# Kernel tuning notes

Measured on AMD Instinct MI355X. Metric: run time of the kernel, lower is better.

The kernel has to match this reference:

```python
import jax, jax.numpy as jnp
import numpy as np

N_FFT = 4096
HOP = 1024
WIN = 300          # wiener_win_len (frames per independent Wiener chunk)
EPS = 1e-10
SCALE_FACTOR = 10.0


def hann(n):
    # torch.hann_window (periodic)
    return 0.5 * (1.0 - jnp.cos(2.0 * jnp.pi * jnp.arange(n) / n))


def stft(x, window):
    # x: (N, C, T) -> complex (N, C, B, F), center=True, reflect pad, onesided
    pad = N_FFT // 2
    xp = jnp.pad(x, ((0, 0), (0, 0), (pad, pad)), mode='reflect')
    n_frames = 1 + (xp.shape[-1] - N_FFT) // HOP
    idx = jnp.arange(n_frames)[:, None] * HOP + jnp.arange(N_FFT)[None, :]
    frames = xp[..., idx] * window                      # (N,C,F,n_fft)
    spec = jnp.fft.rfft(frames, axis=-1)                # (N,C,F,B)
    return jnp.swapaxes(spec, -1, -2)                   # (N,C,B,F)


def istft(spec, window, length):
    # spec: (..., B, F) complex -> (..., length) real; center=True inverse
    frames = jnp.fft.irfft(jnp.swapaxes(spec, -1, -2), n=N_FFT, axis=-1) * window
    n_frames = frames.shape[-2]
    out_len = N_FFT + HOP * (n_frames - 1)
    idx = jnp.arange(n_frames)[:, None] * HOP + jnp.arange(N_FFT)[None, :]
    out = jnp.zeros(frames.shape[:-2] + (out_len,), frames.dtype).at[..., idx].add(frames)
    wsum = jnp.zeros((out_len,), frames.dtype).at[idx].add(
        jnp.broadcast_to(window ** 2, idx.shape))
    out = out / jnp.where(wsum > 1e-11, wsum, 1.0)
    pad = N_FFT // 2
    return out[..., pad:pad + length]


def wiener_chunk(v, x, niter):
    # openunmix.filtering.wiener (softmask=False, residual=False) on one chunk.
    # v: (T, B, C, S) real target magnitudes; x: (T, B, C) complex mix STFT.
    phase = jnp.exp(1j * jnp.angle(x))                  # mixture phase init
    y = (v * phase[..., None]).astype(jnp.complex64)    # (T,B,C,S)
    max_abs = jnp.maximum(1.0, jnp.max(jnp.abs(x)) / SCALE_FACTOR)
    x = x / max_abs
    y = y / max_abs
    C = x.shape[-1]
    reg = np.sqrt(EPS) * jnp.eye(C, dtype=jnp.complex64)
    for _ in range(niter):  # expectation_maximization, one pass per iter
        psd = jnp.mean(jnp.abs(y) ** 2, axis=2)         # (T,B,S) channel-avg PSD
        # spatial covariance per bin/source, normalized by eps + sum_t psd
        R = jnp.einsum('tbcs,tbds->bcds', y, jnp.conj(y))
        R = R / (EPS + jnp.sum(psd, axis=0))[:, None, None, :]
        Cxx = reg + jnp.einsum('tbs,bcds->tbcd', psd.astype(jnp.complex64), R)
        inv = jnp.linalg.inv(Cxx)                       # (T,B,C,C)
        gain = jnp.einsum('bacs,tbcd->tbads', R, inv) * psd[:, :, None, None, :]
        y = jnp.einsum('tbacs,tbc->tbas', gain, x)      # (T,B,C,S)
    return y * max_abs


def setup_inputs() -> dict:
    key = jax.random.key(0)
    k1, k2 = jax.random.split(key)
    audio = jax.random.normal(k1, (2, 2, 613376), dtype=jnp.float32)
    W = jax.random.normal(k2, (4, 2049), dtype=jnp.float32)  # per-target per-bin mask logits
    return {'audio': audio, 'W': W, 'niter': 1}


def reference(audio, W, niter):
    window = hann(N_FFT).astype(audio.dtype)
    mix = stft(audio, window)                           # (N,C,B,F) complex
    X = jnp.abs(mix)                                    # ComplexNorm power=1
    # target models (stand-in: per-bin sigmoid masks); input detached as in torch
    Xd = jax.lax.stop_gradient(X)
    masks = jax.nn.sigmoid(W)                           # (S,B)
    specs = Xd[..., None] * jnp.transpose(masks)[None, None, :, None, :]  # (N,C,B,F,S)
    v = jnp.transpose(specs, (0, 3, 2, 1, 4))           # (N,F,B,C,S)
    xm = jnp.transpose(mix, (0, 3, 2, 1))               # (N,F,B,C)
    N, F, B, C = xm.shape
    S = v.shape[-1]
    n_chunks = F // WIN
    vc = v.reshape(N, n_chunks, WIN, B, C, S)
    xc = xm.reshape(N, n_chunks, WIN, B, C)
    wfun = lambda vv, xx: wiener_chunk(vv, xx, niter)
    yc = jax.vmap(jax.vmap(wfun))(vc, xc)               # (N,chunks,T,B,C,S)
    y = yc.reshape(N, F, B, C, S)
    y = jnp.transpose(y, (0, 4, 3, 2, 1))               # (N,S,C,B,F)
    estimates = istft(y, window, audio.shape[-1])       # (N,S,C,T)
    return estimates
```

## Files before the change

kernel.cpp:

```cpp
#include <hip/hip_runtime.h>
#include <math.h>

#define TLEN 613376
#define OLEN 617472
#define NFR  600
#define NB   2049
#define PI_F  3.14159265358979323846f
#define PI2_F 6.28318530717958647693f
#define PHYS(i) ((i) + ((i) >> 4))

__device__ __forceinline__ float winf(int j) {
  return 0.5f - 0.5f * __cosf(1.5339807878856412e-3f * (float)j);
}

__device__ __forceinline__ float wsum_at(int m) {
  int f_max = m >> 10; if (f_max > 599) f_max = 599;
  int f_min = (m - 3072) >> 10; if (f_min < 0) f_min = 0;
  float ws = 0.f;
  for (int f2 = f_min; f2 <= f_max; ++f2) {
    float w = winf(m - (f2 << 10));
    ws += w * w;
  }
  return (ws > 1e-11f) ? ws : 1.0f;
}

__device__ __forceinline__ float reflect_load(const float* __restrict__ x, int pos) {
  int k = pos - 2048;
  if (k < 0) k = -k;
  else if (k >= TLEN) k = 2 * TLEN - 2 - k;
  return x[k];
}

__device__ __forceinline__ float2 cmul(float2 a, float2 b) {
  return make_float2(a.x * b.x - a.y * b.y, a.x * b.y + a.y * b.x);
}
__device__ __forceinline__ float2 cadd(float2 a, float2 b) { return make_float2(a.x + b.x, a.y + b.y); }
__device__ __forceinline__ float2 csub(float2 a, float2 b) { return make_float2(a.x - b.x, a.y - b.y); }
template<int SGN>
__device__ __forceinline__ float2 muli(float2 a) {
  return (SGN > 0) ? make_float2(-a.y, a.x) : make_float2(a.y, -a.x);
}

template<int SGN>
__device__ __forceinline__ void fft4(float2 v[4]) {
  float2 t0 = cadd(v[0], v[2]), t1 = csub(v[0], v[2]);
  float2 t2 = cadd(v[1], v[3]), t3 = csub(v[1], v[3]);
  float2 it3 = muli<SGN>(t3);
  v[0] = cadd(t0, t2); v[2] = csub(t0, t2);
  v[1] = cadd(t1, it3); v[3] = csub(t1, it3);
}

template<int SGN>
__device__ __forceinline__ void fft8(float2 v[8]) {
  const float C = 0.70710678118654752440f;
  const float s = (SGN > 0) ? 1.0f : -1.0f;
  float2 t0 = cadd(v[0], v[4]), t1 = csub(v[0], v[4]);
  float2 t2 = cadd(v[2], v[6]), t3 = csub(v[2], v[6]);
  float2 e0 = cadd(t0, t2), e2 = csub(t0, t2);
  float2 it3 = muli<SGN>(t3);
  float2 e1 = cadd(t1, it3), e3 = csub(t1, it3);
  t0 = cadd(v[1], v[5]); t1 = csub(v[1], v[5]);
  t2 = cadd(v[3], v[7]); t3 = csub(v[3], v[7]);
  float2 o0 = cadd(t0, t2), o2 = csub(t0, t2);
  it3 = muli<SGN>(t3);
  float2 o1 = cadd(t1, it3), o3 = csub(t1, it3);
  float2 o1w = make_float2(C * (o1.x - s * o1.y), C * (o1.y + s * o1.x));
  float2 o2w = muli<SGN>(o2);
  float2 o3w = make_float2(C * (-o3.x - s * o3.y), C * (-o3.y + s * o3.x));
  v[0] = cadd(e0, o0);  v[4] = csub(e0, o0);
  v[1] = cadd(e1, o1w); v[5] = csub(e1, o1w);
  v[2] = cadd(e2, o2w); v[6] = csub(e2, o2w);
  v[3] = cadd(e3, o3w); v[7] = csub(e3, o3w);
}

template<int SGN>
__device__ __forceinline__ void twiddle8(float2 v[8], float ang) {
  float sn, cs;
  __sincosf((SGN > 0) ? ang : -ang, &sn, &cs);
  float2 w1 = make_float2(cs, sn);
  float2 w = w1;
  v[1] = cmul(v[1], w);
#pragma unroll
  for (int r = 2; r < 8; ++r) { w = cmul(w, w1); v[r] = cmul(v[r], w); }
}

template<int SGN>
__device__ __forceinline__ void fft2048_mid(float2* lds, float2 v[8], int tid) {
  fft8<SGN>(v);
#pragma unroll
  for (int r = 0; r < 8; ++r) { int i = tid * 8 + r; lds[PHYS(i)] = v[r]; }
  __syncthreads();
#pragma unroll
  for (int r = 0; r < 8; ++r) v[r] = lds[PHYS(tid + 256 * r)];
  twiddle8<SGN>(v, PI2_F * (1.0f / 64.0f) * (float)(tid & 7));
  fft8<SGN>(v);
  __syncthreads();
#pragma unroll
  for (int r = 0; r < 8; ++r) { int i = ((tid >> 3) << 6) + (tid & 7) + 8 * r; lds[PHYS(i)] = v[r]; }
  __syncthreads();
#pragma unroll
  for (int r = 0; r < 8; ++r) v[r] = lds[PHYS(tid + 256 * r)];
  twiddle8<SGN>(v, PI2_F * (1.0f / 512.0f) * (float)(tid & 63));
  fft8<SGN>(v);
  __syncthreads();
#pragma unroll
  for (int r = 0; r < 8; ++r) { int i = ((tid >> 6) << 9) + (tid & 63) + 64 * r; lds[PHYS(i)] = v[r]; }
  __syncthreads();
}

template<int SGN>
__device__ __forceinline__ void fft2048_last(const float2* lds, int jj, float2 u[4]) {
#pragma unroll
  for (int r = 0; r < 4; ++r) u[r] = lds[PHYS(jj + 512 * r)];
  float sn, cs;
  float ang = PI2_F * (1.0f / 2048.0f) * (float)jj;
  __sincosf((SGN > 0) ? ang : -ang, &sn, &cs);
  float2 w1 = make_float2(cs, sn);
  float2 w2 = cmul(w1, w1);
  float2 w3 = cmul(w2, w1);
  u[1] = cmul(u[1], w1); u[2] = cmul(u[2], w2); u[3] = cmul(u[3], w3);
  fft4<SGN>(u);
}

__global__ __launch_bounds__(256, 6) void stft_kernel(const float* __restrict__ audio,
                                                      float2* __restrict__ X) {
  __shared__ float2 lds[2176];
  int bid = blockIdx.x;
  int f  = bid % NFR;
  int nc = bid / NFR;
  const float* x = audio + (size_t)nc * TLEN;
  int tid = threadIdx.x;
  int base = f * 1024;
  float2 v[8];
#pragma unroll
  for (int r = 0; r < 8; ++r) {
    int k = tid + 256 * r;
    int j0 = 2 * k;
    v[r] = make_float2(reflect_load(x, base + j0)     * winf(j0),
                       reflect_load(x, base + j0 + 1) * winf(j0 + 1));
  }
  fft2048_mid<-1>(lds, v, tid);
  fft2048_last<-1>(lds, tid,        v);
  fft2048_last<-1>(lds, tid + 256,  v + 4);
  __syncthreads();
#pragma unroll
  for (int r = 0; r < 4; ++r) lds[PHYS(tid + 512 * r)] = v[r];
#pragma unroll
  for (int r = 0; r < 4; ++r) lds[PHYS(tid + 256 + 512 * r)] = v[4 + r];
  __syncthreads();
  float2* out = X + (size_t)bid * NB;
  float sn0, cs0;
  __sincosf(-PI_F * (float)tid * (1.0f / 2048.0f), &sn0, &cs0);
  float2 ph = make_float2(cs0, sn0);
  const float2 rot = make_float2(0.92387953251128675613f, -0.38268343236508977173f);
#pragma unroll
  for (int r = 0; r < 9; ++r) {
    int k = tid + 256 * r;
    if (k <= 2048) {
      float2 Zk = lds[PHYS(k & 2047)];
      float2 Zm = lds[PHYS((2048 - k) & 2047)];
      float Ex = 0.5f * (Zk.x + Zm.x), Ey = 0.5f * (Zk.y - Zm.y);
      float Dx = 0.5f * (Zk.x - Zm.x), Dy = 0.5f * (Zk.y + Zm.y);
      float Ox = Dy, Oy = -Dx;
      out[k] = make_float2(Ex + Ox * ph.x - Oy * ph.y, Ey + Ox * ph.y + Oy * ph.x);
    }
    ph = cmul(ph, rot);
  }
}

__global__ __launch_bounds__(256) void stats_kernel(const float2* __restrict__ X,
                                                    float* __restrict__ stats4,
                                                    unsigned int* __restrict__ maxsq) {
  __shared__ unsigned int sm;
  if (threadIdx.x == 0) sm = 0u;
  __syncthreads();
  int b = blockIdx.x * 256 + threadIdx.x;
  bool ok = (b < NB);
  int g = blockIdx.y;
  int n = g >> 1, chunk = g & 1;
  int t0 = blockIdx.z * 75;
  const float2* X0 = X + ((size_t)(n * 2 + 0) * NFR + chunk * 300 + t0) * NB + (ok ? b : 0);
  const float2* X1 = X + ((size_t)(n * 2 + 1) * NFR + chunk * 300 + t0) * NB + (ok ? b : 0);
  float s00 = 0.f, s11 = 0.f, sre = 0.f, sim = 0.f, lmax = 0.f;
  if (ok) {
    for (int t = 0; t < 75; ++t) {
      float2 a = X0[(size_t)t * NB];
      float2 c = X1[(size_t)t * NB];
      float pa = a.x * a.x + a.y * a.y;
      float pc = c.x * c.x + c.y * c.y;
      s00 += pa; s11 += pc;
      sre += a.x * c.x + a.y * c.y;
      sim += a.y * c.x - a.x * c.y;
      lmax = fmaxf(lmax, fmaxf(pa, pc));
    }
  }
  atomicMax(&sm, __float_as_uint(lmax));
  __syncthreads();
  if (threadIdx.x == 0) atomicMax(&maxsq[g], sm);
  if (ok) {
    float* sp = stats4 + ((size_t)g * NB + b) * 4;
    unsafeAtomicAdd(sp + 0, s00);
    unsafeAtomicAdd(sp + 1, s11);
    unsafeAtomicAdd(sp + 2, sre);
    unsafeAtomicAdd(sp + 3, sim);
  }
}

__global__ __launch_bounds__(256) void alpha_kernel(const float* __restrict__ Wmask,
                                                    const float4* __restrict__ stats4,
                                                    const unsigned int* __restrict__ maxsq,
                                                    float* __restrict__ alpha,
                                                    float* __restrict__ Ksum) {
  int idx = blockIdx.x * 256 + threadIdx.x;
  if (idx >= 4 * NB) return;
  int b = idx % NB;
  int g = idx / NB;
  float ma2 = fmaxf(1.0f, __uint_as_float(maxsq[g]) * 0.01f);
  float4 s4 = stats4[(size_t)g * NB + b];
  float P = 0.5f * (s4.x + s4.y) / ma2;
  float K = 0.f;
#pragma unroll
  for (int s = 0; s < 4; ++s) {
    float mv = 1.0f / (1.0f + expf(-Wmask[s * NB + b]));
    float m2 = mv * mv;
    float a = (m2 * m2) / (1e-10f + m2 * P);
    alpha[(size_t)(g * 4 + s) * NB + b] = a;
    K += a;
  }
  Ksum[(size_t)g * NB + b] = K;
}

__device__ __forceinline__ float2 wiener_eval(int b, const float2* __restrict__ x0row,
                                              const float2* __restrict__ x1row,
                                              const float4* __restrict__ srow,
                                              const float* __restrict__ arow,
                                              const float* __restrict__ krow,
                                              float ima2, int c) {
  float4 s4 = srow[b];
  float g00 = s4.x * ima2, g11 = s4.y * ima2, gre = s4.z * ima2, gim = s4.w * ima2;
  float K = krow[b];
  float as = arow[b];
  float2 x0 = x0row[b], x1 = x1row[b];
  float ph = 0.5f * ((x0.x * x0.x + x0.y * x0.y) + (x1.x * x1.x + x1.y * x1.y)) * ima2;
  float pk = ph * K;
  float M00 = 1e-5f + pk * g00;
  float M11 = 1e-5f + pk * g11;
  float Mre = pk * gre, Mim = pk * gim;
  float det = M00 * M11 - (Mre * Mre + Mim * Mim);
  float sc = ph * as / det;
  float u0x = M11 * x0.x - (Mre * x1.x - Mim * x1.y);
  float u0y = M11 * x0.y - (Mre * x1.y + Mim * x1.x);
  float u1x = M00 * x1.x - (Mre * x0.x + Mim * x0.y);
  float u1y = M00 * x1.y - (Mre * x0.y - Mim * x0.x);
  float wx, wy;
  if (c == 0) {
    wx = g00 * u0x + (gre * u1x - gim * u1y);
    wy = g00 * u0y + (gre * u1y + gim * u1x);
  } else {
    wx = (gre * u0x + gim * u0y) + g11 * u1x;
    wy = (gre * u0y - gim * u0x) + g11 * u1y;
  }
  return make_float2(wx * sc, wy * sc);
}

template<int MODE>
__global__ __launch_bounds__(256, 6) void istft_pass_kernel(const float2* __restrict__ X,
                                                            const float4* __restrict__ stats4,
                                                            const float* __restrict__ alpha,
                                                            const float* __restrict__ Ksum,
                                                            const unsigned int* __restrict__ maxsq,
                                                            float* __restrict__ accum,
                                                            float* __restrict__ out,
                                                            int pass) {
  __shared__ float2 lds[2176];
  int bid = blockIdx.x;
  int fi = bid % 150;
  int plane = bid / 150;
  int c = plane & 1;
  int s = (plane >> 1) & 3;
  int n = plane >> 3;
  int f = 4 * fi + pass;
  int g = n * 2 + (f >= 300 ? 1 : 0);
  int tid = threadIdx.x;
  const float2* x0row = X + ((size_t)(n * 2 + 0) * NFR + f) * NB;
  const float2* x1row = X + ((size_t)(n * 2 + 1) * NFR + f) * NB;
  const float4* srow = stats4 + (size_t)g * NB;
  const float*  arow = alpha + (size_t)(g * 4 + s) * NB;
  const float*  krow = Ksum + (size_t)g * NB;
  float ima2 = 1.0f / fmaxf(1.0f, __uint_as_float(maxsq[g]) * 0.01f);
#pragma unroll
  for (int r = 0; r < 9; ++r) {
    int k = tid + 256 * r;
    if (k <= 2048) lds[k] = wiener_eval(k, x0row, x1row, srow, arow, krow, ima2, c);
  }
  __syncthreads();
  float2 v[8];
  float sn0, cs0;
  __sincosf(PI_F * (float)tid * (1.0f / 2048.0f), &sn0, &cs0);
  float2 ph = make_float2(cs0, sn0);
  const float2 rot = make_float2(0.92387953251128675613f, 0.38268343236508977173f);
#pragma unroll
  for (int r = 0; r < 8; ++r) {
    int k = tid + 256 * r;
    float2 sk = lds[k];
    float2 sv = lds[2048 - k];
    float Ex = 0.5f * (sk.x + sv.x), Ey = 0.5f * (sk.y - sv.y);
    float Dx = 0.5f * (sk.x - sv.x), Dy = 0.5f * (sk.y + sv.y);
    float Ox = Dx * ph.x - Dy * ph.y, Oy = Dx * ph.y + Dy * ph.x;
    v[r] = make_float2(Ex - Oy, Ey + Ox);
    ph = cmul(ph, rot);
  }
  __syncthreads();
  fft2048_mid<1>(lds, v, tid);
  float* acc = accum + (size_t)plane * OLEN + (size_t)f * 1024;
  float* outp = out + (size_t)plane * TLEN;
  const float scale = 1.0f / 2048.0f;
#pragma unroll
  for (int half = 0; half < 2; ++half) {
    int jj = tid + 256 * half;
    float2 u[4];
    fft2048_last<1>(lds, jj, u);
#pragma unroll
    for (int r = 0; r < 4; ++r) {
      int m = jj + 512 * r;
      int j0 = 2 * m;
      float2 val = make_float2(u[r].x * scale * winf(j0),
                               u[r].y * scale * winf(j0 + 1));
      float2* p = (float2*)&acc[j0];
      if (MODE == 0) {
        *p = val;
      } else if (MODE == 1) {
        float2 o = *p; val.x += o.x; val.y += o.y;
        *p = val;
      } else {
        int gm = f * 1024 + j0;
        if (gm < 615424) {
          float2 o = *p; val.x += o.x; val.y += o.y;
          float i0, i1;
          if (gm >= 3072 && gm + 1 < 614400) {
            i0 = 0.66666666666666667f; i1 = i0;
          } else {
            i0 = 1.0f / wsum_at(gm); i1 = 1.0f / wsum_at(gm + 1);
          }
          float2* po = (float2*)&outp[gm - 2048];
          *po = make_float2(val.x * i0, val.y * i1);
        }
      }
    }
  }
  if (MODE == 0 && fi == 149) {
    float* tail = accum + (size_t)plane * OLEN + 614400;
    for (int i = tid; i < OLEN - 614400; i += 256) tail[i] = 0.f;
  }
  if (MODE == 2 && fi == 0) {
    float* accp = accum + (size_t)plane * OLEN;
    for (int m = 2048 + tid; m < 3072; m += 256) {
      outp[m - 2048] = accp[m] / wsum_at(m);
    }
  }
}

extern "C" void kernel_launch(void* const* d_in, const int* in_sizes, int n_in,
                              void* d_out, int out_size, void* d_ws, size_t ws_size,
                              hipStream_t stream) {
  const float* audio = (const float*)d_in[0];
  const float* Wmask = (const float*)d_in[1];
  float* out = (float*)d_out;

  char* ws = (char*)d_ws;
  const size_t off_stats4 = 0;
  const size_t off_maxsq  = 131136;
  const size_t zero_span  = 131200;
  const size_t off_X      = zero_span;
  const size_t off_accum  = off_X + 39340800;
  const size_t off_alpha  = off_accum + 39518208;
  const size_t off_Ksum   = off_alpha + 131136;

  float*        stats4f = (float*)(ws + off_stats4);
  float4*       stats4  = (float4*)(ws + off_stats4);
  unsigned int* maxsq   = (unsigned int*)(ws + off_maxsq);
  float2*       X       = (float2*)(ws + off_X);
  float*        accum   = (float*)(ws + off_accum);
  float*        alpha   = (float*)(ws + off_alpha);
  float*        Ksum    = (float*)(ws + off_Ksum);

  hipMemsetAsync(ws, 0, zero_span, stream);

  stft_kernel<<<2400, 256, 0, stream>>>(audio, X);
  stats_kernel<<<dim3(9, 4, 4), 256, 0, stream>>>(X, stats4f, maxsq);
  alpha_kernel<<<(4 * NB + 255) / 256, 256, 0, stream>>>(Wmask, stats4, maxsq, alpha, Ksum);
  istft_pass_kernel<0><<<2400, 256, 0, stream>>>(X, stats4, alpha, Ksum, maxsq, accum, out, 0);
  istft_pass_kernel<1><<<2400, 256, 0, stream>>>(X, stats4, alpha, Ksum, maxsq, accum, out, 1);
  istft_pass_kernel<1><<<2400, 256, 0, stream>>>(X, stats4, alpha, Ksum, maxsq, accum, out, 2);
  istft_pass_kernel<2><<<2400, 256, 0, stream>>>(X, stats4, alpha, Ksum, maxsq, accum, out, 3);
}
```

Baseline: 220.2 us.

## Precompute source-independent Wiener filter output once in a separate kernel

Moves the per-bin Wiener evaluation out of the iSTFT pass kernels into a dedicated kernel. It computes both channel outputs once per frame and bin, without the per-source alpha factor, and stores them in a new workspace buffer. Each iSTFT block then loads these values and scales them by alpha, instead of recomputing the 2x2 solve for every source and channel. This also removes an LDS staging step and a barrier. In exchange it adds an extra kernel launch and about 39 MB of extra global writes and reads.

```diff
diff --git a/kernel.cpp b/kernel.cpp
--- a/kernel.cpp
+++ b/kernel.cpp
@@ -230,45 +230,48 @@
   Ksum[(size_t)g * NB + b] = K;
 }
 
-__device__ __forceinline__ float2 wiener_eval(int b, const float2* __restrict__ x0row,
-                                              const float2* __restrict__ x1row,
-                                              const float4* __restrict__ srow,
-                                              const float* __restrict__ arow,
-                                              const float* __restrict__ krow,
-                                              float ima2, int c) {
-  float4 s4 = srow[b];
+__global__ __launch_bounds__(256) void wiener_kernel(const float2* __restrict__ X,
+                                                     const float4* __restrict__ stats4,
+                                                     const float* __restrict__ Ksum,
+                                                     const unsigned int* __restrict__ maxsq,
+                                                     float2* __restrict__ Wc) {
+  int idx = blockIdx.x * 256 + threadIdx.x;
+  if (idx >= 4 * 300 * NB) return;
+  int b = idx % NB;
+  int gt = idx / NB;
+  int t = gt % 300;
+  int g = gt / 300;
+  int n = g >> 1, chunk = g & 1;
+  int f = chunk * 300 + t;
+  float ima2 = 1.0f / fmaxf(1.0f, __uint_as_float(maxsq[g]) * 0.01f);
+  float4 s4 = stats4[(size_t)g * NB + b];
   float g00 = s4.x * ima2, g11 = s4.y * ima2, gre = s4.z * ima2, gim = s4.w * ima2;
-  float K = krow[b];
-  float as = arow[b];
-  float2 x0 = x0row[b], x1 = x1row[b];
+  float K = Ksum[(size_t)g * NB + b];
+  float2 x0 = X[((size_t)(n * 2 + 0) * NFR + f) * NB + b];
+  float2 x1 = X[((size_t)(n * 2 + 1) * NFR + f) * NB + b];
   float ph = 0.5f * ((x0.x * x0.x + x0.y * x0.y) + (x1.x * x1.x + x1.y * x1.y)) * ima2;
   float pk = ph * K;
   float M00 = 1e-5f + pk * g00;
   float M11 = 1e-5f + pk * g11;
   float Mre = pk * gre, Mim = pk * gim;
   float det = M00 * M11 - (Mre * Mre + Mim * Mim);
-  float sc = ph * as / det;
+  float sc = ph / det;
   float u0x = M11 * x0.x - (Mre * x1.x - Mim * x1.y);
   float u0y = M11 * x0.y - (Mre * x1.y + Mim * x1.x);
   float u1x = M00 * x1.x - (Mre * x0.x + Mim * x0.y);
   float u1y = M00 * x1.y - (Mre * x0.y - Mim * x0.x);
-  float wx, wy;
-  if (c == 0) {
-    wx = g00 * u0x + (gre * u1x - gim * u1y);
-    wy = g00 * u0y + (gre * u1y + gim * u1x);
-  } else {
-    wx = (gre * u0x + gim * u0y) + g11 * u1x;
-    wy = (gre * u0y - gim * u0x) + g11 * u1y;
-  }
-  return make_float2(wx * sc, wy * sc);
+  float w0x = g00 * u0x + (gre * u1x - gim * u1y);
+  float w0y = g00 * u0y + (gre * u1y + gim * u1x);
+  float w1x = (gre * u0x + gim * u0y) + g11 * u1x;
+  float w1y = (gre * u0y - gim * u0x) + g11 * u1y;
+  float2* out = Wc + ((size_t)(n * NFR + f) * 2) * NB + b;
+  out[0]  = make_float2(w0x * sc, w0y * sc);
+  out[NB] = make_float2(w1x * sc, w1y * sc);
 }
 
 template<int MODE>
-__global__ __launch_bounds__(256, 6) void istft_pass_kernel(const float2* __restrict__ X,
-                                                            const float4* __restrict__ stats4,
+__global__ __launch_bounds__(256, 6) void istft_pass_kernel(const float2* __restrict__ Wc,
                                                             const float* __restrict__ alpha,
-                                                            const float* __restrict__ Ksum,
-                                                            const unsigned int* __restrict__ maxsq,
                                                             float* __restrict__ accum,
                                                             float* __restrict__ out,
                                                             int pass) {
@@ -282,18 +285,8 @@
   int f = 4 * fi + pass;
   int g = n * 2 + (f >= 300 ? 1 : 0);
   int tid = threadIdx.x;
-  const float2* x0row = X + ((size_t)(n * 2 + 0) * NFR + f) * NB;
-  const float2* x1row = X + ((size_t)(n * 2 + 1) * NFR + f) * NB;
-  const float4* srow = stats4 + (size_t)g * NB;
+  const float2* Wrow = Wc + ((size_t)(n * NFR + f) * 2 + c) * NB;
   const float*  arow = alpha + (size_t)(g * 4 + s) * NB;
-  const float*  krow = Ksum + (size_t)g * NB;
-  float ima2 = 1.0f / fmaxf(1.0f, __uint_as_float(maxsq[g]) * 0.01f);
-#pragma unroll
-  for (int r = 0; r < 9; ++r) {
-    int k = tid + 256 * r;
-    if (k <= 2048) lds[k] = wiener_eval(k, x0row, x1row, srow, arow, krow, ima2, c);
-  }
-  __syncthreads();
   float2 v[8];
   float sn0, cs0;
   __sincosf(PI_F * (float)tid * (1.0f / 2048.0f), &sn0, &cs0);
@@ -302,15 +295,17 @@
 #pragma unroll
   for (int r = 0; r < 8; ++r) {
     int k = tid + 256 * r;
-    float2 sk = lds[k];
-    float2 sv = lds[2048 - k];
+    float ak = arow[k];
+    float2 sk = Wrow[k]; sk.x *= ak; sk.y *= ak;
+    int rk = 2048 - k;
+    float am = arow[rk];
+    float2 sv = Wrow[rk]; sv.x *= am; sv.y *= am;
     float Ex = 0.5f * (sk.x + sv.x), Ey = 0.5f * (sk.y - sv.y);
     float Dx = 0.5f * (sk.x - sv.x), Dy = 0.5f * (sk.y + sv.y);
     float Ox = Dx * ph.x - Dy * ph.y, Oy = Dx * ph.y + Dy * ph.x;
     v[r] = make_float2(Ex - Oy, Ey + Ox);
     ph = cmul(ph, rot);
   }
-  __syncthreads();
   fft2048_mid<1>(lds, v, tid);
   float* acc = accum + (size_t)plane * OLEN + (size_t)f * 1024;
   float* outp = out + (size_t)plane * TLEN;
@@ -372,7 +367,8 @@
   const size_t off_maxsq  = 131136;
   const size_t zero_span  = 131200;
   const size_t off_X      = zero_span;
-  const size_t off_accum  = off_X + 39340800;
+  const size_t off_Wc     = off_X + 39340800;
+  const size_t off_accum  = off_Wc + 39340800;
   const size_t off_alpha  = off_accum + 39518208;
   const size_t off_Ksum   = off_alpha + 131136;
 
@@ -380,6 +376,7 @@
   float4*       stats4  = (float4*)(ws + off_stats4);
   unsigned int* maxsq   = (unsigned int*)(ws + off_maxsq);
   float2*       X       = (float2*)(ws + off_X);
+  float2*       Wc      = (float2*)(ws + off_Wc);
   float*        accum   = (float*)(ws + off_accum);
   float*        alpha   = (float*)(ws + off_alpha);
   float*        Ksum    = (float*)(ws + off_Ksum);
@@ -389,8 +386,9 @@
   stft_kernel<<<2400, 256, 0, stream>>>(audio, X);
   stats_kernel<<<dim3(9, 4, 4), 256, 0, stream>>>(X, stats4f, maxsq);
   alpha_kernel<<<(4 * NB + 255) / 256, 256, 0, stream>>>(Wmask, stats4, maxsq, alpha, Ksum);
-  istft_pass_kernel<0><<<2400, 256, 0, stream>>>(X, stats4, alpha, Ksum, maxsq, accum, out, 0);
-  istft_pass_kernel<1><<<2400, 256, 0, stream>>>(X, stats4, alpha, Ksum, maxsq, accum, out, 1);
-  istft_pass_kernel<1><<<2400, 256, 0, stream>>>(X, stats4, alpha, Ksum, maxsq, accum, out, 2);
-  istft_pass_kernel<2><<<2400, 256, 0, stream>>>(X, stats4, alpha, Ksum, maxsq, accum, out, 3);
-}
+  wiener_kernel<<<(4 * 300 * NB + 255) / 256, 256, 0, stream>>>(X, stats4, Ksum, maxsq, Wc);
+  istft_pass_kernel<0><<<2400, 256, 0, stream>>>(Wc, alpha, accum, out, 0);
+  istft_pass_kernel<1><<<2400, 256, 0, stream>>>(Wc, alpha, accum, out, 1);
+  istft_pass_kernel<1><<<2400, 256, 0, stream>>>(Wc, alpha, accum, out, 2);
+  istft_pass_kernel<2><<<2400, 256, 0, stream>>>(Wc, alpha, accum, out, 3);
+}
```

Measured after the change: 206.3 us. 6.3% less time.
